# Kernel optimization log

Measured on AMD Instinct MI355X. Metric: run time of the kernel, lower is better.

## Reference

```python
import jax, jax.numpy as jnp
import numpy as np

B, T, V, D = 4, 2048, 1024, 512


def setup_inputs() -> dict:
    key = jax.random.key(0)
    ks = jax.random.split(key, 6)
    x = jax.random.normal(ks[0], (B, T, V), dtype=jnp.float32)
    decay_logit = jax.random.uniform(ks[1], (), dtype=jnp.float32)
    scale = jnp.ones((), dtype=jnp.float32)
    std = 0.02
    # Linear weights stored as [in, out] so projection is x @ W
    Wq = std * jax.random.normal(ks[2], (V, D), dtype=jnp.float32)
    Wk = std * jax.random.normal(ks[3], (V, D), dtype=jnp.float32)
    Wv = std * jax.random.normal(ks[4], (V, D), dtype=jnp.float32)
    Wo = std * jax.random.normal(ks[5], (D, V), dtype=jnp.float32)
    return {"x": x, "decay_logit": decay_logit, "scale": scale,
            "Wq": Wq, "Wk": Wk, "Wv": Wv, "Wo": Wo}


def reference(x, decay_logit, scale, Wq, Wk, Wv, Wo):
    dtype = x.dtype
    xf = x.astype(jnp.float32)
    q = (xf @ Wq).astype(dtype)  # [B,T,D]
    k = (xf @ Wk).astype(dtype)
    v = (xf @ Wv).astype(dtype)
    scores = jnp.einsum('btd,bsd->bts', q, k)  # [B,T,T]
    decay = jax.nn.sigmoid(decay_logit)
    pos = jnp.arange(T)
    diff = pos[None, :] - pos[:, None]  # diff[i,j] = j - i
    expo = jnp.maximum(diff.astype(jnp.float32) - 1.0, 0.0)
    weights = (decay ** expo) * (diff > 0)  # [T,T]
    scores = scores * weights.astype(dtype)[None, :, :]
    retrieved = jnp.einsum('bts,bsd->btd', scores, v)  # [B,T,D]
    out = (retrieved.astype(jnp.float32) @ Wo).astype(dtype) * scale
    return out
```

## Files before the change

### kernel.cpp

```cpp
#include <hip/hip_runtime.h>
#include <stdint.h>


using bf16u = unsigned short;
using short8 = __attribute__((ext_vector_type(8))) short;
using f32x16 = __attribute__((ext_vector_type(16))) float;

__device__ __forceinline__ unsigned short f2bf(float f) {
  unsigned int u = __float_as_uint(f);
  u += 0x7fffu + ((u >> 16) & 1u);
  return (unsigned short)(u >> 16);
}

__device__ __forceinline__ void gload16(const void* g, void* l) {
  __builtin_amdgcn_global_load_lds(
      (const __attribute__((address_space(1))) void*)g,
      (__attribute__((address_space(3))) void*)l, 16, 0, 0);
}

template<int N> __device__ __forceinline__ void waitvm() {
  if constexpr (N == 0)      asm volatile("s_waitcnt vmcnt(0)" ::: "memory");
  else if constexpr (N == 4) asm volatile("s_waitcnt vmcnt(4)" ::: "memory");
}

#define BK 32

template<int MODE, int TBM, int TBN>
__global__ __launch_bounds__(256, 4)
void gemm_bt(const bf16u* __restrict__ A, const bf16u* __restrict__ Bt,
             void* __restrict__ Cout,
             int K, int ldA, int ldB, int ldC,
             long sA, long sB, long sC,
             int nbx, const float* __restrict__ scal)
{
  constexpr int WR = TBM / 2, WC = TBN / 2;
  constexpr int MF = WR / 32, NF = WC / 32;
  constexpr int RA = TBM / 64, RB = TBN / 64;
  constexpr int L  = RA + RB;

  __shared__ bf16u Al[3][TBM * BK];
  __shared__ bf16u Bl[3][TBN * BK];
  const int z = blockIdx.z;
  A  += (long)z * sA;
  Bt += (long)z * sB;

  const int nwg  = gridDim.x;
  const int orig = blockIdx.x;
  const int q8 = nwg >> 3, r8 = nwg & 7;
  const int xcd = orig & 7, lid = orig >> 3;
  const int wgid = (xcd < r8 ? xcd * (q8 + 1)
                             : r8 * (q8 + 1) + (xcd - r8) * q8) + lid;
  const int by = wgid / nbx, bx = wgid - by * nbx;
  const int bm = by * TBM;
  const int bn = (MODE == 1) ? ((bm >> 7) + bx) * TBN : bx * TBN;
  const int kofsB = (MODE == 3) ? (bm & ~127) : 0;

  const int tid  = threadIdx.x;
  const int wid  = tid >> 6;
  const int lane = tid & 63;
  const int wr = (wid >> 1) * WR;
  const int wc = (wid & 1) * WC;

  f32x16 acc[MF][NF] = {};

  const int base0 = wid * 1024;
  const int lin0  = base0 + lane * 16;
  const int r0row = lin0 >> 6;
  const int c16   = (lin0 >> 4) & 3;
  const int rcol  = (c16 ^ ((r0row >> 1) & 3)) << 3;

  const int nt = K / BK;

  auto stage = [&](int buf, int kk) {
#pragma unroll
    for (int r = 0; r < RA; ++r)
      gload16(A + (long)(bm + r * 64 + r0row) * ldA + kk + rcol,
              (char*)&Al[buf][0] + r * 4096 + base0);
#pragma unroll
    for (int r = 0; r < RB; ++r)
      gload16(Bt + (long)(bn + r * 64 + r0row) * ldB + kofsB + kk + rcol,
              (char*)&Bl[buf][0] + r * 4096 + base0);
  };

  stage(0, 0);
  if (nt > 1) stage(1, BK);

  const int r31 = lane & 31;
  const int hi  = lane >> 5;
  int cur = 0;
  for (int t = 0; t < nt; ++t) {
    if (t + 1 < nt) waitvm<L>(); else waitvm<0>();
    __builtin_amdgcn_s_barrier();
    __builtin_amdgcn_sched_barrier(0);
    if (t + 2 < nt) {
      int nx = cur + 2; if (nx >= 3) nx -= 3;
      stage(nx, (t + 2) * BK);
    }
    short8 af[MF][2], bfr[NF][2];
#pragma unroll
    for (int m = 0; m < MF; ++m) {
      int row = wr + m * 32 + r31;
      int sw = (row >> 1) & 3;
      af[m][0] = *(const short8*)&Al[cur][row * BK + ((hi       ^ sw) << 3)];
      af[m][1] = *(const short8*)&Al[cur][row * BK + (((2 + hi) ^ sw) << 3)];
    }
#pragma unroll
    for (int n = 0; n < NF; ++n) {
      int row = wc + n * 32 + r31;
      int sw = (row >> 1) & 3;
      bfr[n][0] = *(const short8*)&Bl[cur][row * BK + ((hi       ^ sw) << 3)];
      bfr[n][1] = *(const short8*)&Bl[cur][row * BK + (((2 + hi) ^ sw) << 3)];
    }
#pragma unroll
    for (int m = 0; m < MF; ++m)
#pragma unroll
      for (int n = 0; n < NF; ++n) {
        acc[m][n] = __builtin_amdgcn_mfma_f32_32x32x16_bf16(
            af[m][0], bfr[n][0], acc[m][n], 0, 0, 0);
        acc[m][n] = __builtin_amdgcn_mfma_f32_32x32x16_bf16(
            af[m][1], bfr[n][1], acc[m][n], 0, 0, 0);
      }
    ++cur; if (cur == 3) cur = 0;
  }

  float mul = 1.0f, l2d = 0.0f;
  if (MODE == 1) {
    float dlv = scal[0];
    float decay = 1.0f / (1.0f + __expf(-dlv));
    l2d = __log2f(decay);
  } else if (MODE == 2) {
    mul = scal[0];
  }

#pragma unroll
  for (int m = 0; m < MF; ++m) {
#pragma unroll
    for (int n = 0; n < NF; ++n) {
#pragma unroll
      for (int r = 0; r < 16; ++r) {
        int rloc = (r & 3) + 8 * (r >> 2) + 4 * hi;
        int row = bm + wr + m * 32 + rloc;
        int col = bn + wc + n * 32 + r31;
        float val = acc[m][n][r];
        if (MODE == 1) {
          int diff = col - row;
          float w = (diff > 0 && col < 2048)
                        ? exp2f((float)(diff - 1) * l2d) : 0.0f;
          int lc = bx * 128 + (wc + n * 32 + r31);
          ((bf16u*)Cout)[(long)z * sC + (long)row * ldC + lc] = f2bf(val * w);
        } else if (MODE == 2) {
          ((float*)Cout)[(long)z * sC + (long)row * ldC + col] = val * mul;
        } else {
          ((bf16u*)Cout)[(long)z * sC + (long)row * ldC + col] = f2bf(val);
        }
      }
    }
  }
}

__global__ __launch_bounds__(256)
void prep(const float4* __restrict__ x, ushort4* __restrict__ x16o,
          const float* __restrict__ Wq, const float* __restrict__ Wk,
          const float* __restrict__ Wv, const float* __restrict__ Wo,
          bf16u* __restrict__ WqT, bf16u* __restrict__ WkT,
          bf16u* __restrict__ WvT, bf16u* __restrict__ WoT)
{
  __shared__ float t[32][33];
  const int bid = blockIdx.x;
  const int tid = threadIdx.x;
  if (bid < 8192) {
    int i = bid * 256 + tid;
    float4 v = x[i];
    ushort4 o;
    o.x = f2bf(v.x); o.y = f2bf(v.y); o.z = f2bf(v.z); o.w = f2bf(v.w);
    x16o[i] = o;
    return;
  }
  const int wi = bid - 8192;
  const int w  = wi >> 9;
  const int ti = wi & 511;
  const float* in; bf16u* out; int R, C;
  if (w == 0)      { in = Wq; out = WqT; R = 1024; C = 512; }
  else if (w == 1) { in = Wk; out = WkT; R = 1024; C = 512; }
  else if (w == 2) { in = Wv; out = WvT; R = 1024; C = 512; }
  else             { in = Wo; out = WoT; R = 512;  C = 1024; }
  const int nx = C >> 5;
  const int c0 = (ti % nx) * 32, r0 = (ti / nx) * 32;
  const int tx = tid & 31, ty = tid >> 5;
#pragma unroll
  for (int i = 0; i < 4; ++i)
    t[ty + 8 * i][tx] = in[(long)(r0 + ty + 8 * i) * C + c0 + tx];
  __syncthreads();
#pragma unroll
  for (int i = 0; i < 4; ++i)
    out[(long)(c0 + ty + 8 * i) * R + r0 + tx] = f2bf(t[tx][ty + 8 * i]);
}

__global__ void tr16(const bf16u* __restrict__ in, bf16u* __restrict__ out,
                     int R, int C, int ldIn, long sIn, long sOut) {
  __shared__ bf16u t[32][33];
  in  += (long)blockIdx.z * sIn;
  out += (long)blockIdx.z * sOut;
  int c0 = blockIdx.x * 32, r0 = blockIdx.y * 32;
  int tx = threadIdx.x, ty = threadIdx.y;
#pragma unroll
  for (int i = 0; i < 4; ++i)
    t[ty + 8 * i][tx] = in[(long)(r0 + ty + 8 * i) * ldIn + c0 + tx];
  __syncthreads();
#pragma unroll
  for (int i = 0; i < 4; ++i)
    out[(long)(c0 + ty + 8 * i) * R + r0 + tx] = t[tx][ty + 8 * i];
}

extern "C" void kernel_launch(void* const* d_in, const int* in_sizes, int n_in,
                              void* d_out, int out_size, void* d_ws, size_t ws_size,
                              hipStream_t stream) {
  const float* x  = (const float*)d_in[0];
  const float* dl = (const float*)d_in[1];
  const float* sc = (const float*)d_in[2];
  const float* Wq = (const float*)d_in[3];
  const float* Wk = (const float*)d_in[4];
  const float* Wv = (const float*)d_in[5];
  const float* Wo = (const float*)d_in[6];

  const int B = 4, T = 2048, V = 1024, D = 512;
  const long MT = (long)B * T;
  const int QKV = 3 * D;
  const int BAND = 256;

  char* p = (char*)d_ws;
  auto alloc = [&](size_t bytes) { char* r = p; p += bytes; return r; };
  bf16u* x16 = (bf16u*)alloc((size_t)MT * V * 2);
  bf16u* WqT = (bf16u*)alloc((size_t)D * V * 2);
  bf16u* WkT = (bf16u*)alloc((size_t)D * V * 2);
  bf16u* WvT = (bf16u*)alloc((size_t)D * V * 2);
  bf16u* WoT = (bf16u*)alloc((size_t)V * D * 2);
  bf16u* qkv = (bf16u*)alloc((size_t)MT * QKV * 2);
  bf16u* vT  = (bf16u*)alloc((size_t)MT * D * 2 + 4096);
  bf16u* Sb  = (bf16u*)alloc((size_t)B * T * BAND * 2);
  bf16u* R   = (bf16u*)alloc((size_t)MT * D * 2);

  prep<<<dim3(8192 + 2048), 256, 0, stream>>>(
      (const float4*)x, (ushort4*)x16, Wq, Wk, Wv, Wo, WqT, WkT, WvT, WoT);

  gemm_bt<0, 128, 128><<<dim3(64 * 12, 1, 1), 256, 0, stream>>>(
      x16, WqT, qkv, V, V, V, QKV, 0, 0, 0, 12, nullptr);

  tr16<<<dim3(D / 32, T / 32, B), dim3(32, 8), 0, stream>>>(
      qkv + 2 * D, vT, T, D, QKV, (long)T * QKV, (long)D * T);

  gemm_bt<1, 128, 128><<<dim3(16 * 2, 1, B), 256, 0, stream>>>(
      qkv, qkv + D, Sb, D, QKV, QKV, BAND,
      (long)T * QKV, (long)T * QKV, (long)T * BAND, 2, dl);

  gemm_bt<3, 128, 128><<<dim3(16 * 4, 1, B), 256, 0, stream>>>(
      Sb, vT, R, BAND, BAND, T, D,
      (long)T * BAND, (long)1 << 20, (long)T * D, 4, nullptr);

  gemm_bt<2, 128, 128><<<dim3(64 * 8, 1, 1), 256, 0, stream>>>(
      R, WoT, d_out, D, D, D, V, 0, 0, 0, 8, sc);
}
```

Measured before the change: 95.92 us.

## Switch GEMM to 16x16 MFMA with multi-subtile B reuse and double buffering

Rewrites the GEMM kernel to use 16x16x32 bf16 MFMA instead of 32x32x16. Each block now computes NSUB strided column subtiles so A tiles are reused across them, which cuts the grid for the QKV and output projections. The pipeline drops from a triple buffer with explicit vmcnt waits to a double buffer with __syncthreads, and the occupancy hint in launch_bounds is removed. The larger register and LDS footprint per block, fewer blocks, and weaker overlap risk lower occupancy and exposed load latency.

```diff
diff --git a/kernel.cpp b/kernel.cpp
--- a/kernel.cpp
+++ b/kernel.cpp
@@ -4,7 +4,7 @@
 
 using bf16u = unsigned short;
 using short8 = __attribute__((ext_vector_type(8))) short;
-using f32x16 = __attribute__((ext_vector_type(16))) float;
+using f32x4  = __attribute__((ext_vector_type(4))) float;
 
 __device__ __forceinline__ unsigned short f2bf(float f) {
   unsigned int u = __float_as_uint(f);
@@ -18,28 +18,23 @@
       (__attribute__((address_space(3))) void*)l, 16, 0, 0);
 }
 
-template<int N> __device__ __forceinline__ void waitvm() {
-  if constexpr (N == 0)      asm volatile("s_waitcnt vmcnt(0)" ::: "memory");
-  else if constexpr (N == 4) asm volatile("s_waitcnt vmcnt(4)" ::: "memory");
-}
-
 #define BK 32
-
-template<int MODE, int TBM, int TBN>
-__global__ __launch_bounds__(256, 4)
+#define TBM 128
+#define TBN 128
+
+template<int MODE, int NSUB>
+__global__ __launch_bounds__(256)
 void gemm_bt(const bf16u* __restrict__ A, const bf16u* __restrict__ Bt,
              void* __restrict__ Cout,
              int K, int ldA, int ldB, int ldC,
              long sA, long sB, long sC,
              int nbx, const float* __restrict__ scal)
 {
-  constexpr int WR = TBM / 2, WC = TBN / 2;
-  constexpr int MF = WR / 32, NF = WC / 32;
-  constexpr int RA = TBM / 64, RB = TBN / 64;
-  constexpr int L  = RA + RB;
-
-  __shared__ bf16u Al[3][TBM * BK];
-  __shared__ bf16u Bl[3][TBN * BK];
+  constexpr int MF = 4, NF = 4;
+  constexpr int RA = 2, RB = 2;
+
+  __shared__ bf16u Al[2][TBM * BK];
+  __shared__ bf16u Bl[2][NSUB][TBN * BK];
   const int z = blockIdx.z;
   A  += (long)z * sA;
   Bt += (long)z * sB;
@@ -53,15 +48,16 @@
   const int by = wgid / nbx, bx = wgid - by * nbx;
   const int bm = by * TBM;
   const int bn = (MODE == 1) ? ((bm >> 7) + bx) * TBN : bx * TBN;
+  const int sstride = nbx * TBN;
   const int kofsB = (MODE == 3) ? (bm & ~127) : 0;
 
   const int tid  = threadIdx.x;
   const int wid  = tid >> 6;
   const int lane = tid & 63;
-  const int wr = (wid >> 1) * WR;
-  const int wc = (wid & 1) * WC;
-
-  f32x16 acc[MF][NF] = {};
+  const int wr = (wid >> 1) * 64;
+  const int wc = (wid & 1) * 64;
+
+  f32x4 acc[NSUB][MF][NF] = {};
 
   const int base0 = wid * 1024;
   const int lin0  = base0 + lane * 16;
@@ -77,52 +73,48 @@
       gload16(A + (long)(bm + r * 64 + r0row) * ldA + kk + rcol,
               (char*)&Al[buf][0] + r * 4096 + base0);
 #pragma unroll
-    for (int r = 0; r < RB; ++r)
-      gload16(Bt + (long)(bn + r * 64 + r0row) * ldB + kofsB + kk + rcol,
-              (char*)&Bl[buf][0] + r * 4096 + base0);
+    for (int s = 0; s < NSUB; ++s)
+#pragma unroll
+      for (int r = 0; r < RB; ++r)
+        gload16(Bt + (long)(bn + s * sstride + r * 64 + r0row) * ldB + kofsB + kk + rcol,
+                (char*)&Bl[buf][s][0] + r * 4096 + base0);
   };
 
   stage(0, 0);
-  if (nt > 1) stage(1, BK);
-
-  const int r31 = lane & 31;
-  const int hi  = lane >> 5;
+  __syncthreads();
+
+  const int fr = lane & 15;
+  const int kc = lane >> 4;
   int cur = 0;
   for (int t = 0; t < nt; ++t) {
-    if (t + 1 < nt) waitvm<L>(); else waitvm<0>();
-    __builtin_amdgcn_s_barrier();
-    __builtin_amdgcn_sched_barrier(0);
-    if (t + 2 < nt) {
-      int nx = cur + 2; if (nx >= 3) nx -= 3;
-      stage(nx, (t + 2) * BK);
+    if (t + 1 < nt) stage(cur ^ 1, (t + 1) * BK);
+    short8 af[MF];
+#pragma unroll
+    for (int m = 0; m < MF; ++m) {
+      int row = wr + m * 16 + fr;
+      af[m] = *(const short8*)&Al[cur][row * BK + ((kc ^ ((row >> 1) & 3)) << 3)];
     }
-    short8 af[MF][2], bfr[NF][2];
-#pragma unroll
-    for (int m = 0; m < MF; ++m) {
-      int row = wr + m * 32 + r31;
-      int sw = (row >> 1) & 3;
-      af[m][0] = *(const short8*)&Al[cur][row * BK + ((hi       ^ sw) << 3)];
-      af[m][1] = *(const short8*)&Al[cur][row * BK + (((2 + hi) ^ sw) << 3)];
+#pragma unroll
+    for (int s = 0; s < NSUB; ++s) {
+      short8 bfr[NF];
+#pragma unroll
+      for (int n = 0; n < NF; ++n) {
+        int row = wc + n * 16 + fr;
+        bfr[n] = *(const short8*)&Bl[cur][s][row * BK + ((kc ^ ((row >> 1) & 3)) << 3)];
+      }
+#pragma unroll
+      for (int m = 0; m < MF; ++m)
+#pragma unroll
+        for (int n = 0; n < NF; ++n)
+          acc[s][m][n] = __builtin_amdgcn_mfma_f32_16x16x32_bf16(
+              af[m], bfr[n], acc[s][m][n], 0, 0, 0);
     }
-#pragma unroll
-    for (int n = 0; n < NF; ++n) {
-      int row = wc + n * 32 + r31;
-      int sw = (row >> 1) & 3;
-      bfr[n][0] = *(const short8*)&Bl[cur][row * BK + ((hi       ^ sw) << 3)];
-      bfr[n][1] = *(const short8*)&Bl[cur][row * BK + (((2 + hi) ^ sw) << 3)];
-    }
-#pragma unroll
-    for (int m = 0; m < MF; ++m)
-#pragma unroll
-      for (int n = 0; n < NF; ++n) {
-        acc[m][n] = __builtin_amdgcn_mfma_f32_32x32x16_bf16(
-            af[m][0], bfr[n][0], acc[m][n], 0, 0, 0);
-        acc[m][n] = __builtin_amdgcn_mfma_f32_32x32x16_bf16(
-            af[m][1], bfr[n][1], acc[m][n], 0, 0, 0);
-      }
-    ++cur; if (cur == 3) cur = 0;
-  }
-
+    __syncthreads();
+    cur ^= 1;
+  }
+
+  const int cc = lane & 15;
+  const int cr = (lane >> 4) * 4;
   float mul = 1.0f, l2d = 0.0f;
   if (MODE == 1) {
     float dlv = scal[0];
@@ -133,25 +125,27 @@
   }
 
 #pragma unroll
-  for (int m = 0; m < MF; ++m) {
-#pragma unroll
-    for (int n = 0; n < NF; ++n) {
-#pragma unroll
-      for (int r = 0; r < 16; ++r) {
-        int rloc = (r & 3) + 8 * (r >> 2) + 4 * hi;
-        int row = bm + wr + m * 32 + rloc;
-        int col = bn + wc + n * 32 + r31;
-        float val = acc[m][n][r];
-        if (MODE == 1) {
-          int diff = col - row;
-          float w = (diff > 0 && col < 2048)
-                        ? exp2f((float)(diff - 1) * l2d) : 0.0f;
-          int lc = bx * 128 + (wc + n * 32 + r31);
-          ((bf16u*)Cout)[(long)z * sC + (long)row * ldC + lc] = f2bf(val * w);
-        } else if (MODE == 2) {
-          ((float*)Cout)[(long)z * sC + (long)row * ldC + col] = val * mul;
-        } else {
-          ((bf16u*)Cout)[(long)z * sC + (long)row * ldC + col] = f2bf(val);
+  for (int s = 0; s < NSUB; ++s) {
+#pragma unroll
+    for (int m = 0; m < MF; ++m) {
+#pragma unroll
+      for (int n = 0; n < NF; ++n) {
+#pragma unroll
+        for (int j = 0; j < 4; ++j) {
+          int row = bm + wr + m * 16 + cr + j;
+          int col = bn + s * sstride + wc + n * 16 + cc;
+          float val = acc[s][m][n][j];
+          if (MODE == 1) {
+            int diff = col - row;
+            float w = (diff > 0 && col < 2048)
+                          ? exp2f((float)(diff - 1) * l2d) : 0.0f;
+            int lc = bx * 128 + (wc + n * 16 + cc);
+            ((bf16u*)Cout)[(long)z * sC + (long)row * ldC + lc] = f2bf(val * w);
+          } else if (MODE == 2) {
+            ((float*)Cout)[(long)z * sC + (long)row * ldC + col] = val * mul;
+          } else {
+            ((bf16u*)Cout)[(long)z * sC + (long)row * ldC + col] = f2bf(val);
+          }
         }
       }
     }
@@ -243,20 +237,20 @@
   prep<<<dim3(8192 + 2048), 256, 0, stream>>>(
       (const float4*)x, (ushort4*)x16, Wq, Wk, Wv, Wo, WqT, WkT, WvT, WoT);
 
-  gemm_bt<0, 128, 128><<<dim3(64 * 12, 1, 1), 256, 0, stream>>>(
-      x16, WqT, qkv, V, V, V, QKV, 0, 0, 0, 12, nullptr);
+  gemm_bt<0, 3><<<dim3(64 * 4, 1, 1), 256, 0, stream>>>(
+      x16, WqT, qkv, V, V, V, QKV, 0, 0, 0, 4, nullptr);
 
   tr16<<<dim3(D / 32, T / 32, B), dim3(32, 8), 0, stream>>>(
       qkv + 2 * D, vT, T, D, QKV, (long)T * QKV, (long)D * T);
 
-  gemm_bt<1, 128, 128><<<dim3(16 * 2, 1, B), 256, 0, stream>>>(
+  gemm_bt<1, 1><<<dim3(16 * 2, 1, B), 256, 0, stream>>>(
       qkv, qkv + D, Sb, D, QKV, QKV, BAND,
       (long)T * QKV, (long)T * QKV, (long)T * BAND, 2, dl);
 
-  gemm_bt<3, 128, 128><<<dim3(16 * 4, 1, B), 256, 0, stream>>>(
+  gemm_bt<3, 1><<<dim3(16 * 4, 1, B), 256, 0, stream>>>(
       Sb, vT, R, BAND, BAND, T, D,
       (long)T * BAND, (long)1 << 20, (long)T * D, 4, nullptr);
 
-  gemm_bt<2, 128, 128><<<dim3(64 * 8, 1, 1), 256, 0, stream>>>(
-      R, WoT, d_out, D, D, D, V, 0, 0, 0, 8, sc);
-}
+  gemm_bt<2, 2><<<dim3(64 * 4, 1, 1), 256, 0, stream>>>(
+      R, WoT, d_out, D, D, D, V, 0, 0, 0, 4, sc);
+}
```

New measurement: 109.6 us. 14.3% more time.
